# Performance work log

Measured on AMD Instinct MI355X. Metric: run time of the kernel, lower is better.

## Reference

```python
import jax, jax.numpy as jnp
import numpy as np
import math

T, P, L, C, H, NPTS = 243, 17, 4, 128, 8, 4
DH = C // H


def _ln(x, g, b):
    m = jnp.mean(x, axis=-1, keepdims=True)
    v = jnp.mean((x - m) ** 2, axis=-1, keepdims=True)
    return (x - m) * jax.lax.rsqrt(v + 1e-5) * g + b


def _bilinear(v, grid):
    # v: [B, D, Hh, Ww]; grid: [B, Q, Pt, 2] in [-1,1], (x->W, y->H),
    # align_corners=False, zero padding (matches F.grid_sample in MSDeformAttn core)
    B, D, Hh, Ww = v.shape
    x = (grid[..., 0] + 1.0) * (Ww * 0.5) - 0.5
    y = (grid[..., 1] + 1.0) * (Hh * 0.5) - 0.5
    x0 = jnp.floor(x)
    y0 = jnp.floor(y)
    x0i = x0.astype(jnp.int32)
    y0i = y0.astype(jnp.int32)
    x1i = x0i + 1
    y1i = y0i + 1
    wx1 = x - x0
    wx0 = 1.0 - wx1
    wy1 = y - y0
    wy0 = 1.0 - wy1
    vf = v.reshape(B, D, Hh * Ww)
    Q, Pt = x.shape[1], x.shape[2]

    def gather(yi, xi):
        valid = ((yi >= 0) & (yi < Hh) & (xi >= 0) & (xi < Ww)).astype(v.dtype)
        idx = jnp.clip(yi, 0, Hh - 1) * Ww + jnp.clip(xi, 0, Ww - 1)
        g = jnp.take_along_axis(vf, idx.reshape(B, 1, Q * Pt), axis=2).reshape(B, D, Q, Pt)
        return g * valid[:, None]

    return (gather(y0i, x0i) * (wy0 * wx0)[:, None]
            + gather(y0i, x1i) * (wy0 * wx1)[:, None]
            + gather(y1i, x0i) * (wy1 * wx0)[:, None]
            + gather(y1i, x1i) * (wy1 * wx1)[:, None])  # [B, D, Q, Pt]


def _forward(x, ref_points, pe_buf, learn_pos, w_off, b_off, w_attn, b_attn,
             w_val, b_val, w_out, b_out, in_w, in_b, out_w, out_b,
             fc1_w, fc1_b, fc2_w, fc2_b, g1, be1, g2, be2, g3, be3):
    b, t, p, l, c = x.shape  # l = n_levels + 1
    Lq = t * p * L
    x0 = x[..., :1, :]
    xs = x[..., 1:, :].reshape(b, Lq, c)
    # --- subforward_self: norm_1 -> PE(query) -> MSDeformAttn ---
    xn = _ln(xs, g1, be1)
    q = (xn.reshape(b, t, p, L, c) + pe_buf + learn_pos).reshape(b, Lq, c)
    off = (q @ w_off.T + b_off).reshape(b, Lq, H, L, NPTS, 2)
    aw = jax.nn.softmax((q @ w_attn.T + b_attn).reshape(b, Lq, H, L * NPTS), axis=-1)
    aw = aw.reshape(b, Lq, H, L, NPTS)
    ref = jnp.broadcast_to(ref_points[:, :, :, None, :], (b, t, p, L, 2)).reshape(b, Lq, 2)
    normalizer = jnp.array([p, t], dtype=x.dtype)  # (W, H) per level
    loc = ref[:, :, None, None, None, :] + off / normalizer  # [b,Lq,H,L,Pt,2]
    grids = 2.0 * loc - 1.0
    val = (xn @ w_val.T + b_val).reshape(b, t, p, L, H, DH)
    v_maps = val.transpose(3, 0, 4, 5, 1, 2).reshape(L, b * H, DH, t, p)
    g = grids.transpose(3, 0, 2, 1, 4, 5).reshape(L, b * H, Lq, NPTS, 2)
    sampled = jax.vmap(_bilinear)(v_maps, g)  # [L, b*H, DH, Lq, Pt]
    aw_t = aw.transpose(3, 0, 2, 1, 4).reshape(L, b * H, 1, Lq, NPTS)
    o = jnp.sum(sampled * aw_t, axis=(0, 4))  # [b*H, DH, Lq]
    o = o.reshape(b, H, DH, Lq).transpose(0, 3, 1, 2).reshape(b, Lq, c)
    xs = (o @ w_out.T + b_out) + xs
    # --- concat level-0 back, cross (self) MHA over (p*l) tokens per frame ---
    xcat = jnp.concatenate([x0, xs.reshape(b, t, p, L, c)], axis=3).reshape(b * t, p * l, c)
    xn2 = _ln(xcat, g2, be2)
    qkv = xn2 @ in_w.T + in_b
    qh, kh, vh = jnp.split(qkv, 3, axis=-1)
    S = p * l
    qh = qh.reshape(b * t, S, H, DH)
    kh = kh.reshape(b * t, S, H, DH)
    vh = vh.reshape(b * t, S, H, DH)
    att = jax.nn.softmax(jnp.einsum('bqhd,bkhd->bhqk', qh, kh) / math.sqrt(DH), axis=-1)
    ca = jnp.einsum('bhqk,bkhd->bqhd', att, vh).reshape(b * t, S, c) @ out_w.T + out_b
    xcat = ca + xcat
    xr = xcat.reshape(b, t, p, l, c)
    # --- MLP block ---
    h = _ln(xr, g3, be3)
    h = jax.nn.gelu(h @ fc1_w.T + fc1_b, approximate=False) @ fc2_w.T + fc2_b
    return h + xr


def setup_inputs() -> dict:
    key = jax.random.key(0)
    ks = jax.random.split(key, 20)
    B = 2
    s = 0.02
    x = jax.random.normal(ks[0], (B, T, P, L + 1, C), jnp.float32)
    ref_points = jax.random.uniform(ks[1], (B, T, P, 2), dtype=jnp.float32)
    # sinusoidal PE buffer
    pos = np.arange(T, dtype=np.float32)[:, None]
    div = np.exp(np.arange(0, C, 2, dtype=np.float32) * (-math.log(10000.0) / C))
    ang = pos * div  # [T, C//2]
    pe = np.zeros((1, T, P, L, C), np.float32)
    pe[..., 0::2] = np.sin(ang)[None, :, None, None, :]
    pe[..., 1::2] = np.cos(ang)[None, :, None, None, :]
    rn = lambda k, shp: s * jax.random.normal(k, shp, jnp.float32)
    return {
        'x': x, 'ref_points': ref_points,
        'pe_buf': jnp.asarray(pe),
        'learn_pos': rn(ks[2], (1, T, P, L, C)),
        'w_off': rn(ks[3], (H * L * NPTS * 2, C)), 'b_off': rn(ks[4], (H * L * NPTS * 2,)),
        'w_attn': rn(ks[5], (H * L * NPTS, C)), 'b_attn': rn(ks[6], (H * L * NPTS,)),
        'w_val': rn(ks[7], (C, C)), 'b_val': rn(ks[8], (C,)),
        'w_out': rn(ks[9], (C, C)), 'b_out': rn(ks[10], (C,)),
        'in_w': rn(ks[11], (3 * C, C)), 'in_b': rn(ks[12], (3 * C,)),
        'out_w': rn(ks[13], (C, C)), 'out_b': rn(ks[14], (C,)),
        'fc1_w': rn(ks[15], (4 * C, C)), 'fc1_b': rn(ks[16], (4 * C,)),
        'fc2_w': rn(ks[17], (C, 4 * C)), 'fc2_b': rn(ks[18], (C,)),
        'g1': jnp.ones((C,), jnp.float32), 'be1': jnp.zeros((C,), jnp.float32),
        'g2': jnp.ones((C,), jnp.float32), 'be2': jnp.zeros((C,), jnp.float32),
        'g3': jnp.ones((C,), jnp.float32), 'be3': jnp.zeros((C,), jnp.float32),
    }


def reference(x, ref_points, pe_buf, learn_pos, w_off, b_off, w_attn, b_attn,
              w_val, b_val, w_out, b_out, in_w, in_b, out_w, out_b,
              fc1_w, fc1_b, fc2_w, fc2_b, g1, be1, g2, be2, g3, be3):
    return _forward(x, ref_points, pe_buf, learn_pos, w_off, b_off, w_attn, b_attn,
                    w_val, b_val, w_out, b_out, in_w, in_b, out_w, out_b,
                    fc1_w, fc1_b, fc2_w, fc2_b, g1, be1, g2, be2, g3, be3)
```

## Files before the change

kernel.cpp:

```cpp
#include <hip/hip_runtime.h>
#include <math.h>

#define T_ 243
#define P_ 17
#define L_ 4
#define C_ 128
#define H_ 8
#define NPTS_ 4
#define DH_ 16
#define B_ 2
#define LQ (T_*P_*L_)
#define NT1 (B_*LQ)
#define LL (L_+1)
#define S_ (P_*LL)
#define NT2 (B_*T_*P_*LL)

typedef __attribute__((ext_vector_type(8))) short short8v;
typedef __attribute__((ext_vector_type(4))) short short4v;
typedef __attribute__((ext_vector_type(4))) float float4v;

__device__ __forceinline__ unsigned short f2bf(float f){
  union { float f; unsigned u; } un; un.f = f;
  unsigned r = un.u + 0x7FFF + ((un.u >> 16) & 1);
  return (unsigned short)(r >> 16);
}
__device__ __forceinline__ float bf2f(unsigned short u){
  union { unsigned u; float f; } un; un.u = ((unsigned)u) << 16; return un.f;
}
__device__ __forceinline__ void dma16(const unsigned short* g, unsigned short* l){
  __builtin_amdgcn_global_load_lds(
      (const __attribute__((address_space(1))) void*)g,
      (__attribute__((address_space(3))) void*)l, 16, 0, 0);
}

__global__ void k_wcvt(const float* __restrict__ w0, const float* __restrict__ w1,
                       const float* __restrict__ w2, const float* __restrict__ w3,
                       const float* __restrict__ w4, const float* __restrict__ w5,
                       const float* __restrict__ w6, const float* __restrict__ w7,
                       unsigned short* __restrict__ dst){
  int i = blockIdx.x*256 + threadIdx.x;
  if (i >= 278528) return;
  float v;
  if      (i < 32768)  v = w0[i];
  else if (i < 49152)  v = w1[i-32768];
  else if (i < 65536)  v = w2[i-49152];
  else if (i < 81920)  v = w3[i-65536];
  else if (i < 131072) v = w4[i-81920];
  else if (i < 147456) v = w5[i-131072];
  else if (i < 212992) v = w6[i-147456];
  else                 v = w7[i-212992];
  dst[i] = f2bf(v);
}

__global__ __launch_bounds__(256) void k_ln1_q(
    const float* __restrict__ x, const float* __restrict__ pe,
    const float* __restrict__ lpos, const float* __restrict__ g1,
    const float* __restrict__ be1, unsigned short* __restrict__ xn,
    unsigned short* __restrict__ q) {
  int w = threadIdx.x >> 6; int lane = threadIdx.x & 63;
  int i = blockIdx.x*4 + w;
  int c = lane*2;
  int b = i / LQ; int r = i % LQ;
  int t = r / (P_*L_); int rp = r % (P_*L_);
  int p = rp / L_; int lv = rp % L_;
  const float* xrow = x + (((size_t)(b*T_+t)*P_ + p)*LL + 1 + lv)*C_;
  float2 v = *(const float2*)(xrow + c);
  float s1 = v.x + v.y, s2 = v.x*v.x + v.y*v.y;
  #pragma unroll
  for (int d=1; d<64; d<<=1){ s1 += __shfl_xor(s1,d); s2 += __shfl_xor(s2,d); }
  float mean = s1*(1.0f/C_);
  float var  = s2*(1.0f/C_) - mean*mean;
  float inv = rsqrtf(var + 1e-5f);
  float2 gg = *(const float2*)(g1 + c);
  float2 bb = *(const float2*)(be1 + c);
  float xn0 = (v.x - mean)*inv*gg.x + bb.x;
  float xn1 = (v.y - mean)*inv*gg.y + bb.y;
  size_t oi = (size_t)i*C_ + c;
  *(unsigned*)(xn + oi) = (unsigned)f2bf(xn0) | ((unsigned)f2bf(xn1) << 16);
  size_t pidx = (((size_t)t*P_ + p)*L_ + lv)*C_ + c;
  float2 pv = *(const float2*)(pe + pidx);
  float2 lp = *(const float2*)(lpos + pidx);
  *(unsigned*)(q + oi) = (unsigned)f2bf(xn0 + pv.x + lp.x) | ((unsigned)f2bf(xn1 + pv.y + lp.y) << 16);
}

__global__ __launch_bounds__(256) void k_ln(
    const float* __restrict__ in, const float* __restrict__ g,
    const float* __restrict__ be, unsigned short* __restrict__ out, int M){
  int w = threadIdx.x >> 6; int lane = threadIdx.x & 63;
  int i = blockIdx.x*4 + w;
  if (i >= M) return;
  int c = lane*2;
  float2 v = *(const float2*)(in + (size_t)i*C_ + c);
  float s1 = v.x + v.y, s2 = v.x*v.x + v.y*v.y;
  #pragma unroll
  for (int d=1; d<64; d<<=1){ s1 += __shfl_xor(s1,d); s2 += __shfl_xor(s2,d); }
  float mean = s1*(1.0f/C_);
  float var  = s2*(1.0f/C_) - mean*mean;
  float inv = rsqrtf(var + 1e-5f);
  float2 gg = *(const float2*)(g + c);
  float2 bb = *(const float2*)(be + c);
  float o0 = (v.x - mean)*inv*gg.x + bb.x;
  float o1 = (v.y - mean)*inv*gg.y + bb.y;
  *(unsigned*)(out + (size_t)i*C_ + c) = (unsigned)f2bf(o0) | ((unsigned)f2bf(o1) << 16);
}

template<int K, int N, int EPI>
__global__ __launch_bounds__(256) void k_mm(
    const unsigned short* __restrict__ A, const unsigned short* __restrict__ Bw,
    const float* __restrict__ bias, const float* __restrict__ res,
    float* __restrict__ outF, unsigned short* __restrict__ outB,
    const float* __restrict__ xres, int M)
{
  constexpr int NST = K / 128;
  __shared__ unsigned short As[64*128];
  __shared__ unsigned short Bs[128*128];
  int tid = threadIdx.x;
  int lane = tid & 63;
  int w = tid >> 6;
  int lr = lane & 15, kg = lane >> 4;
  int m0 = blockIdx.x * 64;
  int n0 = blockIdx.y * 128;
  int lrow = lane >> 4;
  int lch  = lane & 15;
  float4v acc[8] = {};
  for (int st = 0; st < NST; ++st){
    int kk = st*128;
    if (st) __syncthreads();
    #pragma unroll
    for (int j = 0; j < 4; ++j){
      int rb = w*16 + j*4;
      int srcch = lch ^ ((rb + lrow) & 7);
      dma16(A + (size_t)(m0 + rb + lrow)*K + kk + srcch*8, As + rb*128);
    }
    #pragma unroll
    for (int j = 0; j < 8; ++j){
      int rb = w*32 + j*4;
      int srcch = lch ^ ((rb + lrow) & 7);
      dma16(Bw + (size_t)(n0 + rb + lrow)*K + kk + srcch*8, Bs + rb*128);
    }
    __syncthreads();
    #pragma unroll
    for (int ks = 0; ks < 4; ++ks){
      int cn = ks*4 + kg;
      int arow = w*16 + lr;
      short8v af = *(const short8v*)(As + arow*128 + ((cn ^ (arow & 7)) * 8));
      #pragma unroll
      for (int nf = 0; nf < 8; ++nf){
        int brow = nf*16 + lr;
        short8v bf = *(const short8v*)(Bs + brow*128 + ((cn ^ (brow & 7)) * 8));
        acc[nf] = __builtin_amdgcn_mfma_f32_16x16x32_bf16(af, bf, acc[nf], 0, 0, 0);
      }
    }
  }
  #pragma unroll
  for (int j = 0; j < 4; ++j){
    int gr = m0 + w*16 + kg*4 + j;
    if (gr >= M) continue;
    int b=0,t=0,p=0,lv=0;
    if (EPI == 2){
      b = gr / LQ; int r = gr % LQ;
      t = r / (P_*L_); int rp = r % (P_*L_);
      p = rp / L_; lv = rp % L_;
    }
    #pragma unroll
    for (int nf = 0; nf < 8; ++nf){
      int gc = n0 + nf*16 + lr;
      float v = acc[nf][j] + bias[gc];
      if (EPI == 0) {
        outF[(size_t)gr*N + gc] = v;
      } else if (EPI == 2) {
        size_t xi = ((((size_t)(b*T_+t)*P_ + p)*LL) + 1 + lv)*(size_t)C_ + gc;
        outF[xi] = v + xres[xi];
      } else if (EPI == 3) {
        outF[(size_t)gr*N + gc] = v + res[(size_t)gr*N + gc];
      } else if (EPI == 4) {
        float gv = 0.5f*v*(1.0f + erff(v*0.70710678118654752440f));
        outB[(size_t)gr*N + gc] = f2bf(gv);
      } else if (EPI == 5) {
        outB[(size_t)gr*N + gc] = f2bf(v);
      }
    }
  }
}

__global__ __launch_bounds__(256) void k_sample(
    const unsigned short* __restrict__ off, const unsigned short* __restrict__ awl,
    const float* __restrict__ refp, const unsigned short* __restrict__ vmap,
    unsigned short* __restrict__ o){
  int gid = blockIdx.x*256 + threadIdx.x;
  if (gid >= NT1*H_) return;
  int h = gid & 7; int i = gid >> 3;
  int b = i / LQ; int r = i % LQ;
  int t = r/(P_*L_); int rp = r%(P_*L_); int p = rp/L_;
  size_t rpi = (((size_t)b*T_+t)*P_+p)*2;
  float refx = refp[rpi + 0]*P_ - 0.5f;
  float refy = refp[rpi + 1]*T_ - 0.5f;

  float offv[32];
  {
    const short8v* op8 = (const short8v*)(off + (size_t)i*256 + h*32);
    #pragma unroll
    for (int s=0;s<4;++s){ short8v v = op8[s];
      #pragma unroll
      for (int j=0;j<8;++j) offv[s*8+j] = bf2f((unsigned short)v[j]); }
  }
  float awv[16];
  {
    const short8v* ap8 = (const short8v*)(awl + (size_t)i*128 + h*16);
    #pragma unroll
    for (int s=0;s<2;++s){ short8v v = ap8[s];
      #pragma unroll
      for (int j=0;j<8;++j) awv[s*8+j] = bf2f((unsigned short)v[j]); }
  }
  float m = awv[0];
  #pragma unroll
  for (int k=1;k<16;++k) m = fmaxf(m, awv[k]);
  float sum = 0.f;
  #pragma unroll
  for (int k=0;k<16;++k){ awv[k] = __expf(awv[k]-m); sum += awv[k]; }
  float inv = 1.f/sum;
  #pragma unroll
  for (int k=0;k<16;++k) awv[k] *= inv;

  float acc[16];
  #pragma unroll
  for (int d=0;d<16;++d) acc[d]=0.f;

  #pragma unroll
  for (int lv=0; lv<L_; ++lv){
    const unsigned short* vlv = vmap + ((size_t)b*LQ + lv)*128 + h*16;
    #pragma unroll
    for (int pt=0; pt<NPTS_; ++pt){
      float px = refx + offv[(lv*4+pt)*2+0];
      float py = refy + offv[(lv*4+pt)*2+1];
      float w  = awv[lv*4+pt];
      float fx = floorf(px), fy = floorf(py);
      int x0 = (int)fx, y0 = (int)fy;
      float wx1 = px - fx, wx0 = 1.f - wx1;
      float wy1 = py - fy, wy0 = 1.f - wy1;
      float cw[4] = {w*wy0*wx0, w*wy0*wx1, w*wy1*wx0, w*wy1*wx1};
      int ys[4] = {y0, y0, y0+1, y0+1};
      int xs[4] = {x0, x0+1, x0, x0+1};
      #pragma unroll
      for (int cidx=0; cidx<4; ++cidx){
        int yy = ys[cidx], xx = xs[cidx];
        if (yy>=0 && yy<T_ && xx>=0 && xx<P_){
          const short8v* vp = (const short8v*)(vlv + (size_t)(yy*P_ + xx)*(L_*128));
          short8v v0 = vp[0], v1 = vp[1];
          float wgt = cw[cidx];
          #pragma unroll
          for (int d=0;d<8;++d){
            acc[d]   = fmaf(wgt, bf2f((unsigned short)v0[d]), acc[d]);
            acc[8+d] = fmaf(wgt, bf2f((unsigned short)v1[d]), acc[8+d]);
          }
        }
      }
    }
  }
  short8v o0, o1;
  #pragma unroll
  for (int d=0;d<8;++d){ o0[d] = (short)f2bf(acc[d]); o1[d] = (short)f2bf(acc[8+d]); }
  short8v* op = (short8v*)(o + (size_t)i*C_ + h*DH_);
  op[0] = o0; op[1] = o1;
}

__global__ void k_copy_x0(const float* __restrict__ x, float* __restrict__ xcat){
  size_t idx = (size_t)blockIdx.x*blockDim.x + threadIdx.x;
  const size_t n = (size_t)B_*T_*P_*C_;
  if (idx < n){
    size_t c = idx % C_; size_t btp = idx / C_;
    size_t xi = (btp*LL)*C_ + c;
    xcat[xi] = x[xi];
  }
}

#define AT_WAVE 7232
__global__ __launch_bounds__(128) void k_attn3(const unsigned short* __restrict__ qkv,
                                               unsigned short* __restrict__ ca){
  __shared__ unsigned short alds[2*AT_WAVE];
  int w = threadIdx.x >> 6; int lane = threadIdx.x & 63;
  int bt = blockIdx.x >> 2; int hp = blockIdx.x & 3;
  int h = hp*2 + w;
  unsigned short* Qb = alds + w*AT_WAVE;
  unsigned short* Kb = Qb + 1920;
  unsigned short* Vb = Qb + 3840;
  unsigned short* Pb = Qb + 5568;
  for (int idx = lane; idx < 192; idx += 64){
    int s = idx >> 1; int d0 = (idx & 1)*8;
    short8v qv = {}, kv = {}, vv = {};
    if (s < 85){
      const unsigned short* rp = qkv + ((size_t)(bt*85+s))*384 + h*16 + d0;
      qv = *(const short8v*)(rp);
      kv = *(const short8v*)(rp + 128);
      vv = *(const short8v*)(rp + 256);
    }
    *(short8v*)(Qb + s*20 + d0) = qv;
    *(short8v*)(Kb + s*20 + d0) = kv;
    #pragma unroll
    for (int j=0;j<8;++j) Vb[(d0+j)*108 + s] = (unsigned short)vv[j];
  }
  __syncthreads();
  int g = lane >> 4; int li = lane & 15;
  const short8v zero8 = {};
  #pragma unroll 1
  for (int qt = 0; qt < 6; ++qt){
    short8v qf = zero8;
    if (g < 2) qf = *(const short8v*)(Qb + (qt*16 + li)*20 + g*8);
    float4v sc[6];
    #pragma unroll
    for (int kt = 0; kt < 6; ++kt){
      short8v kf = zero8;
      if (g < 2) kf = *(const short8v*)(Kb + (kt*16 + li)*20 + g*8);
      float4v z = {};
      sc[kt] = __builtin_amdgcn_mfma_f32_16x16x32_bf16(kf, qf, z, 0, 0, 0);
    }
    float m = -1e30f;
    #pragma unroll
    for (int kt = 0; kt < 6; ++kt)
      #pragma unroll
      for (int j = 0; j < 4; ++j){
        float v = sc[kt][j]*0.25f;
        if (kt == 5 && (g*4 + j) >= 5) v = -1e30f;
        sc[kt][j] = v;
        m = fmaxf(m, v);
      }
    m = fmaxf(m, __shfl_xor(m, 16));
    m = fmaxf(m, __shfl_xor(m, 32));
    float sum = 0.f;
    #pragma unroll
    for (int kt = 0; kt < 6; ++kt){
      short4v pf;
      #pragma unroll
      for (int j = 0; j < 4; ++j){
        float e = __expf(sc[kt][j] - m);
        sum += e;
        pf[j] = (short)f2bf(e);
      }
      *(short4v*)(Pb + li*104 + kt*16 + g*4) = pf;
    }
    sum += __shfl_xor(sum, 16);
    sum += __shfl_xor(sum, 32);
    float inv = 1.f/sum;
    float4v oacc = {};
    #pragma unroll
    for (int kt32 = 0; kt32 < 3; ++kt32){
      short8v vf  = *(const short8v*)(Vb + li*108 + kt32*32 + g*8);
      short8v pf8 = *(const short8v*)(Pb + li*104 + kt32*32 + g*8);
      oacc = __builtin_amdgcn_mfma_f32_16x16x32_bf16(vf, pf8, oacc, 0, 0, 0);
    }
    int q = qt*16 + li;
    if (q < 85){
      short4v ov;
      #pragma unroll
      for (int j=0;j<4;++j) ov[j] = (short)f2bf(oacc[j]*inv);
      *(short4v*)(ca + ((size_t)bt*85 + q)*128 + h*16 + g*4) = ov;
    }
  }
}

extern "C" void kernel_launch(void* const* d_in, const int* in_sizes, int n_in,
                              void* d_out, int out_size, void* d_ws, size_t ws_size,
                              hipStream_t stream) {
  (void)in_sizes; (void)n_in; (void)out_size; (void)ws_size;
  const float* x      = (const float*)d_in[0];
  const float* refp   = (const float*)d_in[1];
  const float* pe     = (const float*)d_in[2];
  const float* lpos   = (const float*)d_in[3];
  const float* w_off  = (const float*)d_in[4];
  const float* b_off  = (const float*)d_in[5];
  const float* w_attn = (const float*)d_in[6];
  const float* b_attn = (const float*)d_in[7];
  const float* w_val  = (const float*)d_in[8];
  const float* b_val  = (const float*)d_in[9];
  const float* w_out  = (const float*)d_in[10];
  const float* b_out  = (const float*)d_in[11];
  const float* in_w   = (const float*)d_in[12];
  const float* in_b   = (const float*)d_in[13];
  const float* out_w  = (const float*)d_in[14];
  const float* out_b  = (const float*)d_in[15];
  const float* fc1_w  = (const float*)d_in[16];
  const float* fc1_b  = (const float*)d_in[17];
  const float* fc2_w  = (const float*)d_in[18];
  const float* fc2_b  = (const float*)d_in[19];
  const float* g1     = (const float*)d_in[20];
  const float* be1    = (const float*)d_in[21];
  const float* g2     = (const float*)d_in[22];
  const float* be2    = (const float*)d_in[23];
  const float* g3     = (const float*)d_in[24];
  const float* be3    = (const float*)d_in[25];
  float* out = (float*)d_out;
  char* wsb = (char*)d_ws;

  unsigned short* xn_b  = (unsigned short*)(wsb + 0);
  unsigned short* q_b   = (unsigned short*)(wsb + 8460288);
  unsigned short* off_b = (unsigned short*)(wsb + 16920576);
  unsigned short* aw_b  = (unsigned short*)(wsb + 33841152);
  unsigned short* vm_b  = (unsigned short*)(wsb + 42301440);
  unsigned short* o_b   = (unsigned short*)(wsb + 50761728);
  float*          xcatB = (float*)(wsb + 59222016);
  unsigned short* xn2_b = (unsigned short*)(wsb + 80372736);
  unsigned short* qkv_b = (unsigned short*)(wsb + 90948096);
  unsigned short* wb    = (unsigned short*)(wsb + 122674176);
  unsigned short* ca_b  = (unsigned short*)(wsb + 0);
  unsigned short* ln3_b = (unsigned short*)(wsb + 80372736);
  unsigned short* hid_b = (unsigned short*)(wsb + 16920576);

  unsigned short* wb_off  = wb + 0;
  unsigned short* wb_attn = wb + 32768;
  unsigned short* wb_val  = wb + 49152;
  unsigned short* wb_wout = wb + 65536;
  unsigned short* wb_in   = wb + 81920;
  unsigned short* wb_outw = wb + 131072;
  unsigned short* wb_fc1  = wb + 147456;
  unsigned short* wb_fc2  = wb + 212992;

  const int GM1 = (NT1 + 63)/64;
  const int GM2 = (NT2 + 63)/64;

  hipLaunchKernelGGL(k_wcvt, dim3((278528+255)/256), dim3(256), 0, stream,
                     w_off, w_attn, w_val, w_out, in_w, out_w, fc1_w, fc2_w, wb);
  hipLaunchKernelGGL(k_ln1_q, dim3(NT1/4), dim3(256), 0, stream, x, pe, lpos, g1, be1, xn_b, q_b);
  hipLaunchKernelGGL((k_mm<128,256,5>), dim3(GM1,2), dim3(256), 0, stream,
                     q_b, wb_off, b_off, nullptr, nullptr, off_b, nullptr, NT1);
  hipLaunchKernelGGL((k_mm<128,128,5>), dim3(GM1,1), dim3(256), 0, stream,
                     q_b, wb_attn, b_attn, nullptr, nullptr, aw_b, nullptr, NT1);
  hipLaunchKernelGGL((k_mm<128,128,5>), dim3(GM1,1), dim3(256), 0, stream,
                     xn_b, wb_val, b_val, nullptr, nullptr, vm_b, nullptr, NT1);
  hipLaunchKernelGGL(k_sample, dim3((NT1*H_+255)/256), dim3(256), 0, stream,
                     off_b, aw_b, refp, vm_b, o_b);
  hipLaunchKernelGGL((k_mm<128,128,2>), dim3(GM1,1), dim3(256), 0, stream,
                     o_b, wb_wout, b_out, nullptr, xcatB, nullptr, x, NT1);
  hipLaunchKernelGGL(k_copy_x0, dim3(((size_t)B_*T_*P_*C_+255)/256), dim3(256), 0, stream, x, xcatB);
  hipLaunchKernelGGL(k_ln, dim3((NT2+3)/4), dim3(256), 0, stream, xcatB, g2, be2, xn2_b, NT2);
  hipLaunchKernelGGL((k_mm<128,384,5>), dim3(GM2,3), dim3(256), 0, stream,
                     xn2_b, wb_in, in_b, nullptr, nullptr, qkv_b, nullptr, NT2);
  hipLaunchKernelGGL(k_attn3, dim3(B_*T_*4), dim3(128), 0, stream, qkv_b, ca_b);
  hipLaunchKernelGGL((k_mm<128,128,3>), dim3(GM2,1), dim3(256), 0, stream,
                     ca_b, wb_outw, out_b, xcatB, xcatB, nullptr, nullptr, NT2);
  hipLaunchKernelGGL(k_ln, dim3((NT2+3)/4), dim3(256), 0, stream, xcatB, g3, be3, ln3_b, NT2);
  hipLaunchKernelGGL((k_mm<128,512,4>), dim3(GM2,4), dim3(256), 0, stream,
                     ln3_b, wb_fc1, fc1_b, nullptr, nullptr, hid_b, nullptr, NT2);
  hipLaunchKernelGGL((k_mm<512,128,3>), dim3(GM2,1), dim3(256), 0, stream,
                     hid_b, wb_fc2, fc2_b, xcatB, out, nullptr, nullptr, NT2);
}
```

Before: 222.4 us.

## Load attention Q/K fragments straight into registers and use four heads per block

```diff
diff --git a/kernel.cpp b/kernel.cpp
--- a/kernel.cpp
+++ b/kernel.cpp
@@ -274,45 +274,45 @@
   }
 }
 
-#define AT_WAVE 7232
-__global__ __launch_bounds__(128) void k_attn3(const unsigned short* __restrict__ qkv,
+__global__ __launch_bounds__(256) void k_attn4(const unsigned short* __restrict__ qkv,
                                                unsigned short* __restrict__ ca){
-  __shared__ unsigned short alds[2*AT_WAVE];
+  __shared__ unsigned short alds[4*4992];
   int w = threadIdx.x >> 6; int lane = threadIdx.x & 63;
-  int bt = blockIdx.x >> 2; int hp = blockIdx.x & 3;
-  int h = hp*2 + w;
-  unsigned short* Qb = alds + w*AT_WAVE;
-  unsigned short* Kb = Qb + 1920;
-  unsigned short* Vb = Qb + 3840;
-  unsigned short* Pb = Qb + 5568;
+  int bt = blockIdx.x >> 1; int hh = blockIdx.x & 1;
+  int h = hh*4 + w;
+  unsigned short* Vb = alds + w*4992;
+  unsigned short* Pb = Vb + 1664;
+  const unsigned short* base = qkv + (size_t)bt*85*384 + h*16;
   for (int idx = lane; idx < 192; idx += 64){
     int s = idx >> 1; int d0 = (idx & 1)*8;
-    short8v qv = {}, kv = {}, vv = {};
-    if (s < 85){
-      const unsigned short* rp = qkv + ((size_t)(bt*85+s))*384 + h*16 + d0;
-      qv = *(const short8v*)(rp);
-      kv = *(const short8v*)(rp + 128);
-      vv = *(const short8v*)(rp + 256);
-    }
-    *(short8v*)(Qb + s*20 + d0) = qv;
-    *(short8v*)(Kb + s*20 + d0) = kv;
-    #pragma unroll
-    for (int j=0;j<8;++j) Vb[(d0+j)*108 + s] = (unsigned short)vv[j];
-  }
-  __syncthreads();
+    short8v vv = {};
+    if (s < 85) vv = *(const short8v*)(base + (size_t)s*384 + 256 + d0);
+    #pragma unroll
+    for (int j=0;j<8;++j) Vb[(d0+j)*104 + s] = (unsigned short)vv[j];
+  }
   int g = lane >> 4; int li = lane & 15;
   const short8v zero8 = {};
-  #pragma unroll 1
+  short8v kf[6], qf[6];
+  #pragma unroll
+  for (int kt = 0; kt < 6; ++kt){
+    kf[kt] = zero8;
+    int key = kt*16 + li;
+    if (g < 2 && key < 85) kf[kt] = *(const short8v*)(base + (size_t)key*384 + 128 + g*8);
+  }
+  #pragma unroll
   for (int qt = 0; qt < 6; ++qt){
-    short8v qf = zero8;
-    if (g < 2) qf = *(const short8v*)(Qb + (qt*16 + li)*20 + g*8);
+    qf[qt] = zero8;
+    int q = qt*16 + li;
+    if (g < 2 && q < 85) qf[qt] = *(const short8v*)(base + (size_t)q*384 + g*8);
+  }
+  #pragma unroll 2
+  for (int qt = 0; qt < 6; ++qt){
+    unsigned short* Pq = Pb + (qt & 1)*1664;
     float4v sc[6];
     #pragma unroll
     for (int kt = 0; kt < 6; ++kt){
-      short8v kf = zero8;
-      if (g < 2) kf = *(const short8v*)(Kb + (kt*16 + li)*20 + g*8);
       float4v z = {};
-      sc[kt] = __builtin_amdgcn_mfma_f32_16x16x32_bf16(kf, qf, z, 0, 0, 0);
+      sc[kt] = __builtin_amdgcn_mfma_f32_16x16x32_bf16(kf[kt], qf[qt], z, 0, 0, 0);
     }
     float m = -1e30f;
     #pragma unroll
@@ -336,7 +336,7 @@
         sum += e;
         pf[j] = (short)f2bf(e);
       }
-      *(short4v*)(Pb + li*104 + kt*16 + g*4) = pf;
+      *(short4v*)(Pq + li*104 + kt*16 + g*4) = pf;
     }
     sum += __shfl_xor(sum, 16);
     sum += __shfl_xor(sum, 32);
@@ -344,8 +344,8 @@
     float4v oacc = {};
     #pragma unroll
     for (int kt32 = 0; kt32 < 3; ++kt32){
-      short8v vf  = *(const short8v*)(Vb + li*108 + kt32*32 + g*8);
-      short8v pf8 = *(const short8v*)(Pb + li*104 + kt32*32 + g*8);
+      short8v vf  = *(const short8v*)(Vb + li*104 + kt32*32 + g*8);
+      short8v pf8 = *(const short8v*)(Pq + li*104 + kt32*32 + g*8);
       oacc = __builtin_amdgcn_mfma_f32_16x16x32_bf16(vf, pf8, oacc, 0, 0, 0);
     }
     int q = qt*16 + li;
@@ -434,7 +434,7 @@
   hipLaunchKernelGGL(k_ln, dim3((NT2+3)/4), dim3(256), 0, stream, xcatB, g2, be2, xn2_b, NT2);
   hipLaunchKernelGGL((k_mm<128,384,5>), dim3(GM2,3), dim3(256), 0, stream,
                      xn2_b, wb_in, in_b, nullptr, nullptr, qkv_b, nullptr, NT2);
-  hipLaunchKernelGGL(k_attn3, dim3(B_*T_*4), dim3(128), 0, stream, qkv_b, ca_b);
+  hipLaunchKernelGGL(k_attn4, dim3(B_*T_*2), dim3(256), 0, stream, qkv_b, ca_b);
   hipLaunchKernelGGL((k_mm<128,128,3>), dim3(GM2,1), dim3(256), 0, stream,
                      ca_b, wb_outw, out_b, xcatB, xcatB, nullptr, nullptr, NT2);
   hipLaunchKernelGGL(k_ln, dim3((NT2+3)/4), dim3(256), 0, stream, xcatB, g3, be3, ln3_b, NT2);
```

Result: slower. 260.8 us (+17.3%).
